# Optimization experiments

Hardware: AMD Instinct MI355X
Metric: run time of the kernel (lower is better)

The kernel has to match this reference:

```python
import jax, jax.numpy as jnp
import numpy as np

EMB_DIM = 768
N_HEAD = 12
WIN = (14, 14)  # relative_window_size; seq_len must equal 14*14=196
BATCH = 64
SEQ = WIN[0] * WIN[1]


def _relative_position_index(wh, ww):
    coords = np.stack(np.meshgrid(np.arange(wh), np.arange(ww), indexing='ij'))
    coords = coords.reshape(2, -1)
    rel = coords[:, :, None] - coords[:, None, :]          # [2, S, S]
    rel = rel.transpose(1, 2, 0).astype(np.int32)          # [S, S, 2]
    rel[:, :, 0] += wh - 1
    rel[:, :, 1] += ww - 1
    rel[:, :, 0] *= 2 * ww - 1
    return rel.sum(-1)                                     # [S, S]


def setup_inputs() -> dict:
    key = jax.random.key(0)
    ks = jax.random.split(key, 10)
    d = EMB_DIM
    std = 0.01
    x = jax.random.normal(ks[0], (BATCH, SEQ, d), dtype=jnp.float32)
    Wq = std * jax.random.normal(ks[1], (d, d), dtype=jnp.float32)
    Wk = std * jax.random.normal(ks[2], (d, d), dtype=jnp.float32)
    Wv = std * jax.random.normal(ks[3], (d, d), dtype=jnp.float32)
    Wo = std * jax.random.normal(ks[4], (d, d), dtype=jnp.float32)
    bq = jnp.zeros((d,), jnp.float32)
    bk = jnp.zeros((d,), jnp.float32)
    bv = jnp.zeros((d,), jnp.float32)
    bo = jnp.zeros((d,), jnp.float32)
    n_bias = (2 * WIN[0] - 1) * (2 * WIN[1] - 1)           # 729
    bias_table = std * jax.random.normal(ks[5], (n_bias, N_HEAD), dtype=jnp.float32)
    rel_index = jnp.asarray(_relative_position_index(WIN[0], WIN[1]))  # int32 [S,S]
    return {"x": x, "Wq": Wq, "bq": bq, "Wk": Wk, "bk": bk, "Wv": Wv,
            "bv": bv, "Wo": Wo, "bo": bo, "bias_table": bias_table,
            "rel_index": rel_index}


def reference(x, Wq, bq, Wk, bk, Wv, bv, Wo, bo, bias_table, rel_index):
    B, S, D = x.shape
    H = N_HEAD
    pd = D // H  # projection_dim

    def split_heads(t):
        return t.reshape(B, S, H, pd).transpose(0, 2, 1, 3)  # [B,H,S,pd]

    q = split_heads(x @ Wq + bq)
    k = split_heads(x @ Wk + bk)
    v = split_heads(x @ Wv + bv)

    # scores: [B,H,S,S], scaled by sqrt(projection_dim) as in the source
    score = jnp.einsum('bhqd,bhkd->bhqk', q, k) / jnp.sqrt(jnp.float32(pd))

    # Swin-style relative position bias: gather [S*S] rows -> [1,H,S,S]
    bias = bias_table[rel_index.reshape(-1)].reshape(S, S, H)
    bias = bias.transpose(2, 0, 1)[None]
    score = score + bias

    weight = jax.nn.softmax(score, axis=-1)
    out = jnp.einsum('bhqk,bhkd->bhqd', weight, v)          # [B,H,S,pd]
    out = out.transpose(0, 2, 1, 3).reshape(B, S, D)
    return out @ Wo + bo
```

## Files before the change

### kernel.cpp

```cpp
#include <hip/hip_runtime.h>
#include <hip/hip_bf16.h>


typedef __bf16 bf16x8 __attribute__((ext_vector_type(8)));
typedef __bf16 bf16x4 __attribute__((ext_vector_type(4)));
typedef float  f32x4  __attribute__((ext_vector_type(4)));

#define MROWS 12544
#define DDIM  768
#define NHEAD 12
#define SEQ   196
#define KSTR  72
#define VSTR  232

static __device__ __forceinline__ f32x4 MFMA(bf16x8 a, bf16x8 b, f32x4 c) {
    return __builtin_amdgcn_mfma_f32_16x16x32_bf16(a, b, c, 0, 0, 0);
}

static __device__ __forceinline__ void gload16(const __bf16* g, __bf16* l) {
    __builtin_amdgcn_global_load_lds(
        (const __attribute__((address_space(1))) void*)(g),
        (__attribute__((address_space(3))) void*)(l),
        16, 0, 0);
}

__global__ __launch_bounds__(256) void f2b(const float* __restrict__ in,
                                           __bf16* __restrict__ out) {
    size_t i = ((size_t)blockIdx.x * 256 + threadIdx.x) * 8;
    f32x4 a = *(const f32x4*)&in[i];
    f32x4 b = *(const f32x4*)&in[i + 4];
    bf16x8 o;
    o[0] = (__bf16)a[0]; o[1] = (__bf16)a[1]; o[2] = (__bf16)a[2]; o[3] = (__bf16)a[3];
    o[4] = (__bf16)b[0]; o[5] = (__bf16)b[1]; o[6] = (__bf16)b[2]; o[7] = (__bf16)b[3];
    *(bf16x8*)&out[i] = o;
}

__global__ __launch_bounds__(256) void wtrans(const float* __restrict__ W0, const float* __restrict__ W1,
                                              const float* __restrict__ W2, const float* __restrict__ W3,
                                              __bf16* __restrict__ T0, __bf16* __restrict__ T1,
                                              __bf16* __restrict__ T2, __bf16* __restrict__ T3) {
    const float* Ws[4] = {W0, W1, W2, W3};
    __bf16*      Ts[4] = {T0, T1, T2, T3};
    const float* W = Ws[blockIdx.z];
    __bf16*      T = Ts[blockIdx.z];
    __shared__ __bf16 t[32][33];
    int k0 = blockIdx.x * 32, n0 = blockIdx.y * 32;
    int c = threadIdx.x & 31, r = threadIdx.x >> 5;
#pragma unroll
    for (int i = 0; i < 4; ++i)
        t[r + i * 8][c] = (__bf16)W[(size_t)(k0 + r + i * 8) * DDIM + n0 + c];
    __syncthreads();
#pragma unroll
    for (int i = 0; i < 4; ++i)
        T[(size_t)(n0 + r + i * 8) * DDIM + k0 + c] = t[c][r + i * 8];
}

__global__ __launch_bounds__(256) void bias_pre(const float* __restrict__ table,
                                                const int* __restrict__ rel,
                                                __bf16* __restrict__ biasH) {
    int i = blockIdx.x * 256 + threadIdx.x;
    if (i < NHEAD * SEQ * SEQ) {
        int h = i / (SEQ * SEQ), qk = i - h * (SEQ * SEQ);
        biasH[i] = (__bf16)table[rel[qk] * NHEAD + h];
    }
}

template <typename OutT, int NMAT>
__global__ __launch_bounds__(512, 2) void gemm8p(const __bf16* __restrict__ A,
                                                 const __bf16* __restrict__ Bt,
                                                 const float* __restrict__ bz0,
                                                 const float* __restrict__ bz1,
                                                 const float* __restrict__ bz2,
                                                 OutT* __restrict__ Cz0,
                                                 OutT* __restrict__ Cz1,
                                                 OutT* __restrict__ Cz2,
                                                 int nbn) {
    __shared__ __bf16 As[3][256 * 64];
    __shared__ __bf16 Bs[2][256 * 64];

    const int nwg = gridDim.x, orig = blockIdx.x;
    const int qq = nwg >> 3, r8 = nwg & 7, xcd = orig & 7, lin = orig >> 3;
    const int wg = (xcd < r8 ? xcd * (qq + 1) : r8 * (qq + 1) + (xcd - r8) * qq) + lin;
    const int bm = wg / nbn, bn = wg - bm * nbn;
    const int m0 = bm * 256, n0g = bn * 256;

    const int tid = threadIdx.x, w = tid >> 6, l = tid & 63;
    const int lr = l & 15, lg = l >> 4;
    const int wrow = (w >> 2) * 128;
    const int wcol = (w & 3) * 64;

    const int srow = w * 8 + (l >> 3);
    const int scol = ((l & 7) ^ ((l >> 3) & 7)) * 8;
    const __bf16* gA = A  + (size_t)(m0 + srow) * DDIM + scol;
    const __bf16* gB = Bt + (size_t)(n0g + srow) * DDIM + scol;

#define STAGE_A(slot, h, kt)                                                      \
    do {                                                                          \
        gload16(gA + ((h) * 128 + 0) * DDIM + (kt) * 64,                          \
                &As[slot][(h) * 8192 + 0 + w * 512]);                             \
        gload16(gA + ((h) * 128 + 64) * DDIM + (kt) * 64,                         \
                &As[slot][(h) * 8192 + 4096 + w * 512]);                          \
    } while (0)
#define STAGE_B(slot, h, kt)                                                      \
    do {                                                                          \
        gload16(gB + ((h) * 128 + 0) * DDIM + (kt) * 64,                          \
                &Bs[slot][(h) * 8192 + 0 + w * 512]);                             \
        gload16(gB + ((h) * 128 + 64) * DDIM + (kt) * 64,                         \
                &Bs[slot][(h) * 8192 + 4096 + w * 512]);                          \
    } while (0)

#define AF(slot, mf, ks)                                                          \
    (*(const bf16x8*)&As[slot][(w >> 2) * 8192 + ((mf) * 16 + lr) * 64 +          \
                              ((((ks) * 4 + lg) ^ (lr & 7))) * 8])
#define BF(slot, nf, ks)                                                          \
    (*(const bf16x8*)&Bs[slot][((w & 3) >> 1) * 8192 +                            \
                              ((w & 1) * 64 + (nf) * 16 + lr) * 64 +              \
                              ((((ks) * 4 + lg) ^ (lr & 7))) * 8])

    f32x4 acc[8][4];
#pragma unroll
    for (int i = 0; i < 8; ++i)
#pragma unroll
        for (int j = 0; j < 4; ++j) acc[i][j] = (f32x4){0.f, 0.f, 0.f, 0.f};

    bf16x8 a0, a1, a2, a3;
    bf16x8 bfr00, bfr01, bfr10, bfr11, bfr20, bfr21, bfr30, bfr31;

#define DSLOAD_A(slot, mf0)                                                       \
    a0 = AF(slot, mf0, 0); a1 = AF(slot, mf0, 1);                                 \
    a2 = AF(slot, (mf0) + 1, 0); a3 = AF(slot, (mf0) + 1, 1);
#define DSLOAD_B(slot)                                                            \
    bfr00 = BF(slot, 0, 0); bfr01 = BF(slot, 0, 1);                               \
    bfr10 = BF(slot, 1, 0); bfr11 = BF(slot, 1, 1);                               \
    bfr20 = BF(slot, 2, 0); bfr21 = BF(slot, 2, 1);                               \
    bfr30 = BF(slot, 3, 0); bfr31 = BF(slot, 3, 1);
#define BARRIER_IN()                                                              \
    __builtin_amdgcn_sched_barrier(0);                                            \
    __builtin_amdgcn_s_barrier();                                                 \
    asm volatile("s_waitcnt lgkmcnt(0)" ::: "memory");                            \
    __builtin_amdgcn_sched_barrier(0);                                            \
    __builtin_amdgcn_s_setprio(1);
#define BARRIER_OUT()                                                             \
    __builtin_amdgcn_s_setprio(0);                                                \
    __builtin_amdgcn_sched_barrier(0);                                            \
    __builtin_amdgcn_s_barrier();                                                 \
    __builtin_amdgcn_sched_barrier(0);
#define MFMACL(mf0)                                                               \
    acc[mf0][0] = MFMA(a0, bfr00, acc[mf0][0]);                                   \
    acc[mf0][0] = MFMA(a1, bfr01, acc[mf0][0]);                                   \
    acc[(mf0) + 1][0] = MFMA(a2, bfr00, acc[(mf0) + 1][0]);                       \
    acc[(mf0) + 1][0] = MFMA(a3, bfr01, acc[(mf0) + 1][0]);                       \
    acc[mf0][1] = MFMA(a0, bfr10, acc[mf0][1]);                                   \
    acc[mf0][1] = MFMA(a1, bfr11, acc[mf0][1]);                                   \
    acc[(mf0) + 1][1] = MFMA(a2, bfr10, acc[(mf0) + 1][1]);                       \
    acc[(mf0) + 1][1] = MFMA(a3, bfr11, acc[(mf0) + 1][1]);                       \
    acc[mf0][2] = MFMA(a0, bfr20, acc[mf0][2]);                                   \
    acc[mf0][2] = MFMA(a1, bfr21, acc[mf0][2]);                                   \
    acc[(mf0) + 1][2] = MFMA(a2, bfr20, acc[(mf0) + 1][2]);                       \
    acc[(mf0) + 1][2] = MFMA(a3, bfr21, acc[(mf0) + 1][2]);                       \
    acc[mf0][3] = MFMA(a0, bfr30, acc[mf0][3]);                                   \
    acc[mf0][3] = MFMA(a1, bfr31, acc[mf0][3]);                                   \
    acc[(mf0) + 1][3] = MFMA(a2, bfr30, acc[(mf0) + 1][3]);                       \
    acc[(mf0) + 1][3] = MFMA(a3, bfr31, acc[(mf0) + 1][3]);

    STAGE_A(0, 0, 0); STAGE_A(0, 1, 0); STAGE_B(0, 0, 0); STAGE_B(0, 1, 0);
    STAGE_A(1, 0, 1); STAGE_A(1, 1, 1); STAGE_B(1, 0, 1); STAGE_B(1, 1, 1);
    asm volatile("s_waitcnt vmcnt(8)" ::: "memory");
    __builtin_amdgcn_s_barrier();
    __builtin_amdgcn_sched_barrier(0);

#pragma unroll
    for (int i = 0; i < 6; ++i) {
        const int s0 = (2 * i) % 3, s1 = (2 * i + 1) % 3, s2 = (2 * i + 2) % 3;
        DSLOAD_A(s0, 0); DSLOAD_B(0);
        if (i < 5) STAGE_A(s2, 0, 2 * i + 2);
        BARRIER_IN(); MFMACL(0); BARRIER_OUT();
        DSLOAD_A(s0, 2);
        if (i < 5) STAGE_A(s2, 1, 2 * i + 2);
        BARRIER_IN(); MFMACL(2); BARRIER_OUT();
        DSLOAD_A(s0, 4);
        if (i < 5) STAGE_B(0, 0, 2 * i + 2);
        BARRIER_IN(); MFMACL(4); BARRIER_OUT();
        DSLOAD_A(s0, 6);
        if (i < 5) {
            STAGE_B(0, 1, 2 * i + 2);
            asm volatile("s_waitcnt vmcnt(8)" ::: "memory");
        } else {
            asm volatile("s_waitcnt vmcnt(0)" ::: "memory");
        }
        BARRIER_IN(); MFMACL(6); BARRIER_OUT();
        DSLOAD_A(s1, 0); DSLOAD_B(1);
        if (i < 5) STAGE_A(s0, 0, 2 * i + 3);
        BARRIER_IN(); MFMACL(0); BARRIER_OUT();
        DSLOAD_A(s1, 2);
        if (i < 5) STAGE_A(s0, 1, 2 * i + 3);
        BARRIER_IN(); MFMACL(2); BARRIER_OUT();
        DSLOAD_A(s1, 4);
        if (i < 5) STAGE_B(1, 0, 2 * i + 3);
        BARRIER_IN(); MFMACL(4); BARRIER_OUT();
        DSLOAD_A(s1, 6);
        if (i < 5) {
            STAGE_B(1, 1, 2 * i + 3);
            asm volatile("s_waitcnt vmcnt(8)" ::: "memory");
        }
        BARRIER_IN(); MFMACL(6); BARRIER_OUT();
    }

    const int mat = (NMAT == 1) ? 0 : (n0g / DDIM);
    const int colbase = n0g - mat * DDIM + wcol;
    const float* bz = (mat == 0) ? bz0 : (mat == 1 ? bz1 : bz2);
    OutT* Cc = (mat == 0) ? Cz0 : (mat == 1 ? Cz1 : Cz2);
#pragma unroll
    for (int nf = 0; nf < 4; ++nf) {
        const int col = colbase + nf * 16 + lr;
        const float bb = bz[col];
#pragma unroll
        for (int mf = 0; mf < 8; ++mf) {
            const int row = m0 + wrow + mf * 16 + lg * 4;
#pragma unroll
            for (int r2 = 0; r2 < 4; ++r2)
                Cc[(size_t)(row + r2) * DDIM + col] = (OutT)(acc[mf][nf][r2] + bb);
        }
    }
#undef STAGE_A
#undef STAGE_B
#undef AF
#undef BF
#undef DSLOAD_A
#undef DSLOAD_B
#undef BARRIER_IN
#undef BARRIER_OUT
#undef MFMACL
}

__global__ __launch_bounds__(512, 1) void attn_kernel(const __bf16* __restrict__ Qg,
                                                      const __bf16* __restrict__ Kg,
                                                      const __bf16* __restrict__ Vg,
                                                      const __bf16* __restrict__ biasH,
                                                      __bf16* __restrict__ Og) {
    __shared__ __bf16 Ksm[208 * KSTR];
    __shared__ __bf16 Vts[64 * VSTR];
    __shared__ __bf16 Psm[8 * 16 * VSTR];

    const int b = blockIdx.x, h = blockIdx.y;
    const int tid = threadIdx.x, w = tid >> 6, l = tid & 63;
    const int lr = l & 15, lg = l >> 4;
    const size_t base = (size_t)(b * SEQ) * DDIM + h * 64;
    const __bf16* Kb = Kg + base;
    const __bf16* Vb = Vg + base;
    const __bf16* Qb = Qg + base;
    const __bf16* bh = biasH + (size_t)h * (SEQ * SEQ);

    for (int c = tid; c < SEQ * 8; c += 512) {
        int kk = c >> 3, d8 = (c & 7) << 3;
        *(bf16x8*)&Ksm[kk * KSTR + d8] = *(const bf16x8*)&Kb[(size_t)kk * DDIM + d8];
    }
    for (int c = tid; c < 12 * 9; c += 512) {
        int kk = SEQ + c / 9, d8 = (c % 9) * 8;
        *(uint4*)&Ksm[kk * KSTR + d8] = make_uint4(0u, 0u, 0u, 0u);
    }
    for (int c = tid; c < SEQ * 8; c += 512) {
        int kk = c >> 3, d8 = (c & 7) << 3;
        bf16x8 vv = *(const bf16x8*)&Vb[(size_t)kk * DDIM + d8];
#pragma unroll
        for (int j = 0; j < 8; ++j) Vts[(d8 + j) * VSTR + kk] = vv[j];
    }
    for (int c = tid; c < 64 * 28; c += 512)
        Vts[(c / 28) * VSTR + SEQ + (c % 28)] = (__bf16)0.f;
    __bf16* Pw = &Psm[w * 16 * VSTR];
    for (int c = l; c < 256; c += 64)
        Pw[(c >> 4) * VSTR + 208 + (c & 15)] = (__bf16)0.f;
    __syncthreads();

    for (int qt = w; qt < 13; qt += 8) {
        const int q0 = qt * 16;
        const int q = q0 + lr;
        const int qrow = min(q, SEQ - 1);
        bf16x8 bq0 = *(const bf16x8*)&Qb[(size_t)qrow * DDIM + lg * 8];
        bf16x8 bq1 = *(const bf16x8*)&Qb[(size_t)qrow * DDIM + 32 + lg * 8];

        f32x4 oa[4];
#pragma unroll
        for (int i = 0; i < 4; ++i) oa[i] = (f32x4){0.f, 0.f, 0.f, 0.f};

        f32x4 sc1[8];
        __builtin_amdgcn_s_setprio(1);
#pragma unroll
        for (int tt = 0; tt < 8; ++tt) {
            bf16x8 kf0 = *(const bf16x8*)&Ksm[(tt * 16 + lr) * KSTR + lg * 8];
            bf16x8 kf1 = *(const bf16x8*)&Ksm[(tt * 16 + lr) * KSTR + 32 + lg * 8];
            f32x4 a = {0.f, 0.f, 0.f, 0.f};
            a = MFMA(kf0, bq0, a);
            a = MFMA(kf1, bq1, a);
            sc1[tt] = a;
        }
        __builtin_amdgcn_s_setprio(0);

        float mx = -1e30f;
#pragma unroll
        for (int tt = 0; tt < 8; ++tt) {
            bf16x4 b4 = *(const bf16x4*)&bh[(size_t)qrow * SEQ + tt * 16 + lg * 4];
#pragma unroll
            for (int r = 0; r < 4; ++r) {
                float v = sc1[tt][r] * 0.125f + (float)b4[r];
                sc1[tt][r] = v;
                mx = fmaxf(mx, v);
            }
        }
        mx = fmaxf(mx, __shfl_xor(mx, 16));
        mx = fmaxf(mx, __shfl_xor(mx, 32));
        float m_run = mx;
        float ps = 0.f;
#pragma unroll
        for (int tt = 0; tt < 8; ++tt) {
            bf16x4 pk;
#pragma unroll
            for (int r = 0; r < 4; ++r) {
                float p = __expf(sc1[tt][r] - m_run);
                ps += p;
                pk[r] = (__bf16)p;
            }
            *(bf16x4*)&Pw[lr * VSTR + tt * 16 + lg * 4] = pk;
        }
        ps += __shfl_xor(ps, 16);
        ps += __shfl_xor(ps, 32);
        float s_run = ps;

        f32x4 sc2[5];
        __builtin_amdgcn_s_setprio(1);
#pragma unroll
        for (int tt = 0; tt < 5; ++tt) {
            const int t = 8 + tt;
            bf16x8 kf0 = *(const bf16x8*)&Ksm[(t * 16 + lr) * KSTR + lg * 8];
            bf16x8 kf1 = *(const bf16x8*)&Ksm[(t * 16 + lr) * KSTR + 32 + lg * 8];
            f32x4 a = {0.f, 0.f, 0.f, 0.f};
            a = MFMA(kf0, bq0, a);
            a = MFMA(kf1, bq1, a);
            sc2[tt] = a;
        }
        __builtin_amdgcn_s_setprio(0);

        float mc2 = -1e30f;
#pragma unroll
        for (int tt = 0; tt < 5; ++tt) {
            const int t = 8 + tt;
            const bool val4 = (t < 12) || (lg == 0);
            float bb[4] = {0.f, 0.f, 0.f, 0.f};
            if (val4) {
                bf16x4 b4 = *(const bf16x4*)&bh[(size_t)qrow * SEQ + t * 16 + lg * 4];
#pragma unroll
                for (int r = 0; r < 4; ++r) bb[r] = (float)b4[r];
            }
#pragma unroll
            for (int r = 0; r < 4; ++r) {
                float v = val4 ? (sc2[tt][r] * 0.125f + bb[r]) : -1e30f;
                sc2[tt][r] = v;
                mc2 = fmaxf(mc2, v);
            }
        }
        mc2 = fmaxf(mc2, __shfl_xor(mc2, 16));
        mc2 = fmaxf(mc2, __shfl_xor(mc2, 32));

        __builtin_amdgcn_s_setprio(1);
#pragma unroll
        for (int kt = 0; kt < 4; ++kt) {
            bf16x8 pf = *(const bf16x8*)&Pw[lr * VSTR + kt * 32 + lg * 8];
#pragma unroll
            for (int nt = 0; nt < 4; ++nt) {
                bf16x8 vf = *(const bf16x8*)&Vts[(nt * 16 + lr) * VSTR + kt * 32 + lg * 8];
                oa[nt] = MFMA(vf, pf, oa[nt]);
            }
        }
        __builtin_amdgcn_s_setprio(0);

        const float mnew = fmaxf(m_run, mc2);
        const float fsc = __expf(m_run - mnew);
        m_run = mnew;
        s_run *= fsc;
#pragma unroll
        for (int i = 0; i < 4; ++i)
#pragma unroll
            for (int r = 0; r < 4; ++r) oa[i][r] *= fsc;
        ps = 0.f;
#pragma unroll
        for (int tt = 0; tt < 5; ++tt) {
            bf16x4 pk;
#pragma unroll
            for (int r = 0; r < 4; ++r) {
                float p = __expf(sc2[tt][r] - m_run);
                ps += p;
                pk[r] = (__bf16)p;
            }
            *(bf16x4*)&Pw[lr * VSTR + (8 + tt) * 16 + lg * 4] = pk;
        }
        ps += __shfl_xor(ps, 16);
        ps += __shfl_xor(ps, 32);
        s_run += ps;

        __builtin_amdgcn_s_setprio(1);
#pragma unroll
        for (int kt = 4; kt < 7; ++kt) {
            bf16x8 pf = *(const bf16x8*)&Pw[lr * VSTR + kt * 32 + lg * 8];
#pragma unroll
            for (int nt = 0; nt < 4; ++nt) {
                bf16x8 vf = *(const bf16x8*)&Vts[(nt * 16 + lr) * VSTR + kt * 32 + lg * 8];
                oa[nt] = MFMA(vf, pf, oa[nt]);
            }
        }
        __builtin_amdgcn_s_setprio(0);

        const float inv = 1.f / s_run;
        if (q < SEQ) {
#pragma unroll
            for (int nt = 0; nt < 4; ++nt) {
                bf16x4 ok;
#pragma unroll
                for (int r = 0; r < 4; ++r) ok[r] = (__bf16)(oa[nt][r] * inv);
                *(bf16x4*)&Og[(size_t)(b * SEQ + q) * DDIM + h * 64 + nt * 16 + lg * 4] = ok;
            }
        }
    }
}

extern "C" void kernel_launch(void* const* d_in, const int* in_sizes, int n_in,
                              void* d_out, int out_size, void* d_ws, size_t ws_size,
                              hipStream_t stream) {
    const float* x     = (const float*)d_in[0];
    const float* Wq    = (const float*)d_in[1];
    const float* bq    = (const float*)d_in[2];
    const float* Wk    = (const float*)d_in[3];
    const float* bk    = (const float*)d_in[4];
    const float* Wv    = (const float*)d_in[5];
    const float* bv    = (const float*)d_in[6];
    const float* Wo    = (const float*)d_in[7];
    const float* bo    = (const float*)d_in[8];
    const float* table = (const float*)d_in[9];
    const int*   rel   = (const int*)d_in[10];
    float* out = (float*)d_out;

    char* ws = (char*)d_ws;
    auto alloc = [&](size_t bytes) {
        char* p = ws;
        ws += (bytes + 255) & ~(size_t)255;
        return p;
    };
    const size_t mat = (size_t)MROWS * DDIM * sizeof(__bf16);
    __bf16* xb    = (__bf16*)alloc(mat);
    __bf16* Tqkv  = (__bf16*)alloc((size_t)3 * DDIM * DDIM * 2);
    __bf16* To    = (__bf16*)alloc((size_t)DDIM * DDIM * 2);
    __bf16* Qb    = (__bf16*)alloc(mat);
    __bf16* Kb    = (__bf16*)alloc(mat);
    __bf16* Vb    = (__bf16*)alloc(mat);
    __bf16* AO    = (__bf16*)alloc(mat);
    __bf16* biasH = (__bf16*)alloc((size_t)NHEAD * SEQ * SEQ * 2);

    f2b<<<dim3(4704), 256, 0, stream>>>(x, xb);
    wtrans<<<dim3(24, 24, 4), 256, 0, stream>>>(Wq, Wk, Wv, Wo,
                                                Tqkv, Tqkv + (size_t)DDIM * DDIM,
                                                Tqkv + (size_t)2 * DDIM * DDIM, To);
    bias_pre<<<dim3(1801), 256, 0, stream>>>(table, rel, biasH);

    gemm8p<__bf16, 3><<<dim3(441), 512, 0, stream>>>(xb, Tqkv, bq, bk, bv,
                                                     Qb, Kb, Vb, 9);
    attn_kernel<<<dim3(64, 12), 512, 0, stream>>>(Qb, Kb, Vb, biasH, AO);
    gemm8p<float, 1><<<dim3(147), 512, 0, stream>>>(AO, To, bo, bo, bo,
                                                    out, out, out, 3);
}
```

Baseline: 161.2 us.

## Fold softmax scale into Wq, swizzle K in LDS, and prefetch bias rows

The 1/sqrt(64) score scale is folded into the transposed Wq and its bias, which removes a multiply per score in attention. The K tile in LDS drops its padded stride for a compact XOR-swizzled 64-wide layout. The V transpose store order is rotated per thread to spread LDS bank conflicts. All 13 relative-bias vectors are loaded up front into registers, and an over-read guard of 1 KB is added to the bias buffer, at the cost of extra register pressure.

```diff
diff --git a/kernel.cpp b/kernel.cpp
--- a/kernel.cpp
+++ b/kernel.cpp
@@ -10,7 +10,6 @@
 #define DDIM  768
 #define NHEAD 12
 #define SEQ   196
-#define KSTR  72
 #define VSTR  232
 
 static __device__ __forceinline__ f32x4 MFMA(bf16x8 a, bf16x8 b, f32x4 c) {
@@ -43,12 +42,13 @@
     __bf16*      Ts[4] = {T0, T1, T2, T3};
     const float* W = Ws[blockIdx.z];
     __bf16*      T = Ts[blockIdx.z];
+    const float s = (blockIdx.z == 0) ? 0.125f : 1.0f;
     __shared__ __bf16 t[32][33];
     int k0 = blockIdx.x * 32, n0 = blockIdx.y * 32;
     int c = threadIdx.x & 31, r = threadIdx.x >> 5;
 #pragma unroll
     for (int i = 0; i < 4; ++i)
-        t[r + i * 8][c] = (__bf16)W[(size_t)(k0 + r + i * 8) * DDIM + n0 + c];
+        t[r + i * 8][c] = (__bf16)(W[(size_t)(k0 + r + i * 8) * DDIM + n0 + c] * s);
     __syncthreads();
 #pragma unroll
     for (int i = 0; i < 4; ++i)
@@ -210,10 +210,11 @@
     const int colbase = n0g - mat * DDIM + wcol;
     const float* bz = (mat == 0) ? bz0 : (mat == 1 ? bz1 : bz2);
     OutT* Cc = (mat == 0) ? Cz0 : (mat == 1 ? Cz1 : Cz2);
+    const float bsc = (NMAT == 3 && mat == 0) ? 0.125f : 1.0f;
 #pragma unroll
     for (int nf = 0; nf < 4; ++nf) {
         const int col = colbase + nf * 16 + lr;
-        const float bb = bz[col];
+        const float bb = bz[col] * bsc;
 #pragma unroll
         for (int mf = 0; mf < 8; ++mf) {
             const int row = m0 + wrow + mf * 16 + lg * 4;
@@ -238,7 +239,7 @@
                                                       const __bf16* __restrict__ Vg,
                                                       const __bf16* __restrict__ biasH,
                                                       __bf16* __restrict__ Og) {
-    __shared__ __bf16 Ksm[208 * KSTR];
+    __shared__ __bf16 Ksm[196 * 64];
     __shared__ __bf16 Vts[64 * VSTR];
     __shared__ __bf16 Psm[8 * 16 * VSTR];
 
@@ -252,18 +253,18 @@
     const __bf16* bh = biasH + (size_t)h * (SEQ * SEQ);
 
     for (int c = tid; c < SEQ * 8; c += 512) {
-        int kk = c >> 3, d8 = (c & 7) << 3;
-        *(bf16x8*)&Ksm[kk * KSTR + d8] = *(const bf16x8*)&Kb[(size_t)kk * DDIM + d8];
-    }
-    for (int c = tid; c < 12 * 9; c += 512) {
-        int kk = SEQ + c / 9, d8 = (c % 9) * 8;
-        *(uint4*)&Ksm[kk * KSTR + d8] = make_uint4(0u, 0u, 0u, 0u);
+        int kk = c >> 3, ch = c & 7;
+        *(bf16x8*)&Ksm[kk * 64 + ((ch ^ (kk & 7)) << 3)] =
+            *(const bf16x8*)&Kb[(size_t)kk * DDIM + (ch << 3)];
     }
     for (int c = tid; c < SEQ * 8; c += 512) {
-        int kk = c >> 3, d8 = (c & 7) << 3;
+        int kk = c >> 3, a = c & 7, d8 = a << 3;
         bf16x8 vv = *(const bf16x8*)&Vb[(size_t)kk * DDIM + d8];
 #pragma unroll
-        for (int j = 0; j < 8; ++j) Vts[(d8 + j) * VSTR + kk] = vv[j];
+        for (int jj = 0; jj < 8; ++jj) {
+            int j = (jj + a) & 7;
+            Vts[(d8 + j) * VSTR + kk] = vv[j];
+        }
     }
     for (int c = tid; c < 64 * 28; c += 512)
         Vts[(c / 28) * VSTR + SEQ + (c % 28)] = (__bf16)0.f;
@@ -272,6 +273,8 @@
         Pw[(c >> 4) * VSTR + 208 + (c & 15)] = (__bf16)0.f;
     __syncthreads();
 
+#define KF(row, ch) (*(const bf16x8*)&Ksm[(row) * 64 + (((ch) ^ ((row) & 7)) << 3)])
+
     for (int qt = w; qt < 13; qt += 8) {
         const int q0 = qt * 16;
         const int q = q0 + lr;
@@ -279,6 +282,11 @@
         bf16x8 bq0 = *(const bf16x8*)&Qb[(size_t)qrow * DDIM + lg * 8];
         bf16x8 bq1 = *(const bf16x8*)&Qb[(size_t)qrow * DDIM + 32 + lg * 8];
 
+        bf16x4 bb4[13];
+#pragma unroll
+        for (int t = 0; t < 13; ++t)
+            bb4[t] = *(const bf16x4*)&bh[(size_t)qrow * SEQ + t * 16 + lg * 4];
+
         f32x4 oa[4];
 #pragma unroll
         for (int i = 0; i < 4; ++i) oa[i] = (f32x4){0.f, 0.f, 0.f, 0.f};
@@ -287,8 +295,9 @@
         __builtin_amdgcn_s_setprio(1);
 #pragma unroll
         for (int tt = 0; tt < 8; ++tt) {
-            bf16x8 kf0 = *(const bf16x8*)&Ksm[(tt * 16 + lr) * KSTR + lg * 8];
-            bf16x8 kf1 = *(const bf16x8*)&Ksm[(tt * 16 + lr) * KSTR + 32 + lg * 8];
+            const int krow = tt * 16 + lr;
+            bf16x8 kf0 = KF(krow, lg);
+            bf16x8 kf1 = KF(krow, 4 + lg);
             f32x4 a = {0.f, 0.f, 0.f, 0.f};
             a = MFMA(kf0, bq0, a);
             a = MFMA(kf1, bq1, a);
@@ -299,10 +308,9 @@
         float mx = -1e30f;
 #pragma unroll
         for (int tt = 0; tt < 8; ++tt) {
-            bf16x4 b4 = *(const bf16x4*)&bh[(size_t)qrow * SEQ + tt * 16 + lg * 4];
 #pragma unroll
             for (int r = 0; r < 4; ++r) {
-                float v = sc1[tt][r] * 0.125f + (float)b4[r];
+                float v = sc1[tt][r] + (float)bb4[tt][r];
                 sc1[tt][r] = v;
                 mx = fmaxf(mx, v);
             }
@@ -330,9 +338,9 @@
         __builtin_amdgcn_s_setprio(1);
 #pragma unroll
         for (int tt = 0; tt < 5; ++tt) {
-            const int t = 8 + tt;
-            bf16x8 kf0 = *(const bf16x8*)&Ksm[(t * 16 + lr) * KSTR + lg * 8];
-            bf16x8 kf1 = *(const bf16x8*)&Ksm[(t * 16 + lr) * KSTR + 32 + lg * 8];
+            const int krow = min((8 + tt) * 16 + lr, SEQ - 1);
+            bf16x8 kf0 = KF(krow, lg);
+            bf16x8 kf1 = KF(krow, 4 + lg);
             f32x4 a = {0.f, 0.f, 0.f, 0.f};
             a = MFMA(kf0, bq0, a);
             a = MFMA(kf1, bq1, a);
@@ -345,15 +353,9 @@
         for (int tt = 0; tt < 5; ++tt) {
             const int t = 8 + tt;
             const bool val4 = (t < 12) || (lg == 0);
-            float bb[4] = {0.f, 0.f, 0.f, 0.f};
-            if (val4) {
-                bf16x4 b4 = *(const bf16x4*)&bh[(size_t)qrow * SEQ + t * 16 + lg * 4];
-#pragma unroll
-                for (int r = 0; r < 4; ++r) bb[r] = (float)b4[r];
-            }
 #pragma unroll
             for (int r = 0; r < 4; ++r) {
-                float v = val4 ? (sc2[tt][r] * 0.125f + bb[r]) : -1e30f;
+                float v = val4 ? (sc2[tt][r] + (float)bb4[t][r]) : -1e30f;
                 sc2[tt][r] = v;
                 mc2 = fmaxf(mc2, v);
             }
@@ -420,6 +422,7 @@
             }
         }
     }
+#undef KF
 }
 
 extern "C" void kernel_launch(void* const* d_in, const int* in_sizes, int n_in,
@@ -452,7 +455,7 @@
     __bf16* Kb    = (__bf16*)alloc(mat);
     __bf16* Vb    = (__bf16*)alloc(mat);
     __bf16* AO    = (__bf16*)alloc(mat);
-    __bf16* biasH = (__bf16*)alloc((size_t)NHEAD * SEQ * SEQ * 2);
+    __bf16* biasH = (__bf16*)alloc((size_t)NHEAD * SEQ * SEQ * 2 + 1024);
 
     f2b<<<dim3(4704), 256, 0, stream>>>(x, xb);
     wtrans<<<dim3(24, 24, 4), 256, 0, stream>>>(Wq, Wk, Wv, Wo,
```

Result: slower. 166.3 us (+3.2%).
